# Optimization experiments

Measured on AMD Instinct MI355X. Metric: run time of the kernel, lower is better.

## Reference

```python
import jax, jax.numpy as jnp
import numpy as np

B, S, H = 4, 4096, 768
NB = 16            # n_blocks (first factor)
BSZ = H // NB      # 48, block size
LN_EPS = 1e-12


def setup_inputs() -> dict:
    key = jax.random.key(0)
    ks = jax.random.split(key, 6)
    hidden_states = jax.random.normal(ks[0], (B, S, H), dtype=jnp.float32)
    # Monarch factors: B1 has NB blocks of (BSZ,BSZ); B2 has BSZ blocks of (NB,NB)
    w1_blocks = jax.random.normal(ks[1], (NB, BSZ, BSZ), dtype=jnp.float32) / np.sqrt(BSZ)
    w2_blocks = jax.random.normal(ks[2], (BSZ, NB, NB), dtype=jnp.float32) / np.sqrt(NB)
    gate_w = jax.random.normal(ks[3], (H, H), dtype=jnp.float32) / np.sqrt(H)
    gate_b = jnp.zeros((H,), dtype=jnp.float32)
    out_w = jax.random.normal(ks[4], (H, H), dtype=jnp.float32) / np.sqrt(H)
    out_b = jnp.zeros((H,), dtype=jnp.float32)
    ln_gamma = jnp.ones((H,), dtype=jnp.float32)
    ln_beta = jnp.zeros((H,), dtype=jnp.float32)
    return {
        "hidden_states": hidden_states,
        "w1_blocks": w1_blocks,
        "w2_blocks": w2_blocks,
        "gate_w": gate_w,
        "gate_b": gate_b,
        "out_w": out_w,
        "out_b": out_b,
        "ln_gamma": ln_gamma,
        "ln_beta": ln_beta,
    }


def _monarch(x, w1, w2):
    # x: [B, S, H]; Monarch product P B2 P B1 applied to last dim.
    b, s, h = x.shape
    y = x.reshape(b, s, NB, BSZ)
    y = jnp.einsum('bski,kij->bskj', y, w1)      # block-diag (NB blocks of BSZxBSZ)
    y = jnp.swapaxes(y, -1, -2)                  # permute: [B,S,BSZ,NB]
    y = jnp.einsum('bsqi,qij->bsqj', y, w2)      # block-diag (BSZ blocks of NBxNB)
    y = jnp.swapaxes(y, -1, -2)                  # permute back: [B,S,NB,BSZ]
    return y.reshape(b, s, h)


def _layernorm(x, gamma, beta, eps):
    mu = jnp.mean(x, axis=-1, keepdims=True)
    var = jnp.mean(jnp.square(x - mu), axis=-1, keepdims=True)
    return (x - mu) * jax.lax.rsqrt(var + eps) * gamma + beta


def reference(hidden_states, w1_blocks, w2_blocks, gate_w, gate_b,
              out_w, out_b, ln_gamma, ln_beta):
    residual = hidden_states
    mixed = _monarch(hidden_states, w1_blocks, w2_blocks)
    gate = jax.nn.sigmoid(hidden_states @ gate_w.T + gate_b)
    h = mixed * gate
    h = h @ out_w.T + out_b
    # dropout is identity in eval / p=0
    return _layernorm(h + residual, ln_gamma, ln_beta, LN_EPS)
```

## Files before the change

kernel.cpp:

```cpp
#include <hip/hip_runtime.h>
#include <hip/hip_bf16.h>
#include <stdint.h>

#define HD 768

typedef __attribute__((ext_vector_type(8))) short bf16x8;
typedef __attribute__((ext_vector_type(4))) float f32x4;

__device__ inline unsigned short f2bf(float f) {
  union { float f; unsigned int u; } v; v.f = f;
  return (unsigned short)((v.u + 0x7fffu + ((v.u >> 16) & 1u)) >> 16);
}
__device__ inline float bf2f(unsigned short u) {
  union { unsigned int uu; float f; } v; v.uu = ((unsigned int)u) << 16;
  return v.f;
}

#define LGKM(N) { asm volatile("s_waitcnt lgkmcnt(" #N ")" ::: "memory"); __builtin_amdgcn_sched_barrier(0); }
#define VMC(N) { asm volatile("s_waitcnt vmcnt(" #N ")" ::: "memory"); __builtin_amdgcn_sched_barrier(0); }

__global__ void prep_kernel(const float* __restrict__ gw, const float* __restrict__ ow,
                            const float* __restrict__ w1, const float* __restrict__ w2,
                            unsigned short* __restrict__ Gpk,
                            unsigned short* __restrict__ Opk,
                            unsigned short* __restrict__ w1f,
                            unsigned short* __restrict__ w2f) {
  int bid = blockIdx.x;
  if (bid < 576) {
    const float* src = (bid < 288) ? gw : ow;
    unsigned short* dst = (bid < 288) ? Gpk : Opk;
    int r = ((bid < 288) ? bid : bid - 288) * 256 + threadIdx.x;
    int lane = r & 63;
    int ks = (r >> 6) % 24;
    int nt = r / (24 * 64);
    int n = nt * 16 + (lane & 15);
    int k = ks * 32 + (lane >> 4) * 8;
    bf16x8 pack;
#pragma unroll
    for (int j = 0; j < 8; ++j) pack[j] = (short)f2bf(src[(size_t)n * HD + k + j]);
    *(bf16x8*)(dst + (size_t)r * 8) = pack;
  } else if (bid < 600) {
    int e = (bid - 576) * 256 + threadIdx.x;
    int lane = e & 63, fi = e >> 6;
    int ks = fi & 1, nt = (fi >> 1) % 3, k = fi / 6;
    int lrr = lane & 15, lgg = lane >> 4;
    int q = nt * 16 + lrr;
    bf16x8 pack;
#pragma unroll
    for (int j = 0; j < 8; ++j) {
      int kk = ks * 32 + lgg * 8 + j;
      float v = (kk < 48) ? w1[(k * 48 + kk) * 48 + q] : 0.0f;
      pack[j] = (short)f2bf(v);
    }
    *(bf16x8*)(w1f + (size_t)e * 8) = pack;
  } else {
    int e = (bid - 600) * 256 + threadIdx.x;
    int lane = e & 63, q = e >> 6;
    int lrr = lane & 15, lgg = lane >> 4;
    bf16x8 pack;
#pragma unroll
    for (int j = 0; j < 8; ++j) {
      int kk = lgg * 8 + j;
      float v = (kk < 16) ? w2[(q * 16 + kk) * 16 + lrr] : 0.0f;
      pack[j] = (short)f2bf(v);
    }
    *(bf16x8*)(w2f + (size_t)e * 8) = pack;
  }
}

__global__ __launch_bounds__(512, 1)
void fused_kernel(const float* __restrict__ x,
                  const unsigned short* __restrict__ Gpk,
                  const unsigned short* __restrict__ Opk,
                  const unsigned short* __restrict__ w1f,
                  const unsigned short* __restrict__ w2f,
                  const float* __restrict__ gate_b,
                  const float* __restrict__ out_b,
                  const float* __restrict__ gamma,
                  const float* __restrict__ beta,
                  float* __restrict__ out) {
  __shared__ __align__(16) unsigned char tile[98304];
  __shared__ __align__(16) unsigned char scratch[49152];
  __shared__ float psum[64][8];
  __shared__ float psq[64][8];

  const int tid = threadIdx.x, lane = tid & 63, wid = tid >> 6;
  const int lr = lane & 15, lg = lane >> 4;
  const size_t m0 = (size_t)blockIdx.x * 64;

  float gbv[6], obv[6];
#pragma unroll
  for (int nt = 0; nt < 6; ++nt) {
    int col = wid * 96 + nt * 16 + lr;
    gbv[nt] = gate_b[col];
    obv[nt] = out_b[col];
  }

  {
    const float4* xs = (const float4*)x + m0 * 192;
#pragma unroll
    for (int p = 0; p < 24; ++p) {
      int id = p * 512 + tid;
      float4 v = xs[id];
      int row = id / 192, c4 = id - row * 192;
      uint2 u;
      u.x = (unsigned int)f2bf(v.x) | ((unsigned int)f2bf(v.y) << 16);
      u.y = (unsigned int)f2bf(v.z) | ((unsigned int)f2bf(v.w) << 16);
      *(uint2*)(tile + row * 1536 + ((c4 * 8) ^ ((row & 7) << 4))) = u;
    }
  }
  __syncthreads();

  const int sx0 = (lg * 16) ^ ((lr & 7) << 4);
  const unsigned char* baA0 = tile + lr * 1536 + sx0;
  const unsigned char* baA1 = tile + lr * 1536 + (sx0 ^ 64);
  const unsigned short* gB = Gpk + ((size_t)(wid * 6) * 24 * 64 + lane) * 8;
  const unsigned short* oB = Opk + ((size_t)(wid * 6) * 24 * 64 + lane) * 8;

  bf16x8 aF0[4], aF1[4];
  bf16x8 bP[12], bQ[12];

#define LOAD_B(BB, KT, BR) { _Pragma("unroll") for (int nt = 0; nt < 6; ++nt) { \
      BR[nt * 2 + 0] = *(const bf16x8*)((BB) + nt * 12288 + ((KT) * 2 + 0) * 512); \
      BR[nt * 2 + 1] = *(const bf16x8*)((BB) + nt * 12288 + ((KT) * 2 + 1) * 512); } }
#define RD_A(KT) { _Pragma("unroll") for (int mt = 0; mt < 4; ++mt) { \
      aF0[mt] = *(const bf16x8*)(baA0 + mt * 24576 + (KT) * 128); \
      aF1[mt] = *(const bf16x8*)(baA1 + mt * 24576 + (KT) * 128); } }
#define MM48(ACC, BR) { __builtin_amdgcn_s_setprio(1); \
    _Pragma("unroll") for (int mt = 0; mt < 4; ++mt) \
    _Pragma("unroll") for (int nt = 0; nt < 6; ++nt) { \
      ACC[mt][nt] = __builtin_amdgcn_mfma_f32_16x16x32_bf16(aF0[mt], BR[nt * 2 + 0], ACC[mt][nt], 0, 0, 0); \
      ACC[mt][nt] = __builtin_amdgcn_mfma_f32_16x16x32_bf16(aF1[mt], BR[nt * 2 + 1], ACC[mt][nt], 0, 0, 0); } \
    __builtin_amdgcn_s_setprio(0); }
#define GEMM_LOOP(BB, ACC) { \
    LOAD_B(BB, 0, bP); \
    _Pragma("unroll 1") \
    for (int kt = 0; kt < 10; kt += 2) { \
      LOAD_B(BB, kt + 1, bQ); RD_A(kt); LGKM(0); VMC(12); MM48(ACC, bP); \
      LOAD_B(BB, kt + 2, bP); RD_A(kt + 1); LGKM(0); VMC(12); MM48(ACC, bQ); \
    } \
    LOAD_B(BB, 11, bQ); RD_A(10); LGKM(0); VMC(12); MM48(ACC, bP); \
    RD_A(11); LGKM(0); VMC(0); MM48(ACC, bQ); }

  f32x4 accG[4][6];
#pragma unroll
  for (int mt = 0; mt < 4; ++mt)
#pragma unroll
    for (int nt = 0; nt < 6; ++nt) accG[mt][nt] = (f32x4){0, 0, 0, 0};
  GEMM_LOOP(gB, accG);

  f32x4 accO[4][6];

#define MONARCH_HALF(H) { \
     \
    _Pragma("unroll") for (int kb = 0; kb < 2; ++kb) { \
      const int k = wid * 2 + kb; \
      const unsigned short* wf = w1f + (size_t)(k * 6) * 512 + lane * 8; \
      bf16x8 w1b0 = *(const bf16x8*)(wf + 0 * 512); \
      bf16x8 w1b1 = *(const bf16x8*)(wf + 1 * 512); \
      bf16x8 w1b2 = *(const bf16x8*)(wf + 2 * 512); \
      bf16x8 w1b3 = *(const bf16x8*)(wf + 3 * 512); \
      bf16x8 w1b4 = *(const bf16x8*)(wf + 4 * 512); \
      bf16x8 w1b5 = *(const bf16x8*)(wf + 5 * 512); \
      _Pragma("unroll") for (int mtl = 0; mtl < 2; ++mtl) { \
        const int row = (H) * 32 + mtl * 16 + lr; \
        const int rsw = (lr & 7) << 4; \
        bf16x8 a0 = *(const bf16x8*)(tile + row * 1536 + ((k * 96 + lg * 16) ^ rsw)); \
        bf16x8 a1 = (bf16x8){0, 0, 0, 0, 0, 0, 0, 0}; \
        if (lg < 2) a1 = *(const bf16x8*)(tile + row * 1536 + ((k * 96 + 64 + lg * 16) ^ rsw)); \
        f32x4 c0 = {0,0,0,0}, c1 = {0,0,0,0}, c2 = {0,0,0,0}; \
        c0 = __builtin_amdgcn_mfma_f32_16x16x32_bf16(a0, w1b0, c0, 0, 0, 0); \
        c0 = __builtin_amdgcn_mfma_f32_16x16x32_bf16(a1, w1b1, c0, 0, 0, 0); \
        c1 = __builtin_amdgcn_mfma_f32_16x16x32_bf16(a0, w1b2, c1, 0, 0, 0); \
        c1 = __builtin_amdgcn_mfma_f32_16x16x32_bf16(a1, w1b3, c1, 0, 0, 0); \
        c2 = __builtin_amdgcn_mfma_f32_16x16x32_bf16(a0, w1b4, c2, 0, 0, 0); \
        c2 = __builtin_amdgcn_mfma_f32_16x16x32_bf16(a1, w1b5, c2, 0, 0, 0); \
        _Pragma("unroll") for (int i = 0; i < 4; ++i) { \
          int rl = mtl * 16 + lg * 4 + i; \
          int zsw = (rl & 7) << 4; \
          *(unsigned short*)(scratch + ((rl * 1536 + 0 * 512 + lr * 32 + k * 2) ^ zsw)) = f2bf(c0[i]); \
          *(unsigned short*)(scratch + ((rl * 1536 + 1 * 512 + lr * 32 + k * 2) ^ zsw)) = f2bf(c1[i]); \
          *(unsigned short*)(scratch + ((rl * 1536 + 2 * 512 + lr * 32 + k * 2) ^ zsw)) = f2bf(c2[i]); } } } \
    __syncthreads(); \
     \
    { unsigned int upk[2][4][3]; \
    _Pragma("unroll") for (int qq = 0; qq < 6; ++qq) { \
      const int q = wid * 6 + qq; \
      bf16x8 bw = *(const bf16x8*)(w2f + (size_t)q * 512 + lane * 8); \
      _Pragma("unroll") for (int mtl = 0; mtl < 2; ++mtl) { \
        int rl = mtl * 16 + lr; \
        bf16x8 a = (bf16x8){0, 0, 0, 0, 0, 0, 0, 0}; \
        if (lg < 2) a = *(const bf16x8*)(scratch + ((rl * 1536 + q * 32 + lg * 16) ^ ((rl & 7) << 4))); \
        f32x4 c = {0, 0, 0, 0}; \
        c = __builtin_amdgcn_mfma_f32_16x16x32_bf16(a, bw, c, 0, 0, 0); \
        _Pragma("unroll") for (int i = 0; i < 4; ++i) { \
          unsigned int h = (unsigned int)f2bf(c[i]); \
          if (qq & 1) upk[mtl][i][qq >> 1] |= (h << 16); \
          else        upk[mtl][i][qq >> 1] = h; } } } \
    __syncthreads();   \
     \
    _Pragma("unroll") for (int mtl = 0; mtl < 2; ++mtl) \
    _Pragma("unroll") for (int i = 0; i < 4; ++i) { \
      int rl = mtl * 16 + lg * 4 + i; \
      int base = rl * 1536 + lr * 96 + wid * 12; \
      int msw = (rl & 7) << 4; \
      _Pragma("unroll") for (int p = 0; p < 3; ++p) \
        *(unsigned int*)(scratch + ((base + p * 4) ^ msw)) = upk[mtl][i][p]; } } \
    __syncthreads(); \
     \
    _Pragma("unroll") for (int mtl = 0; mtl < 2; ++mtl) \
    _Pragma("unroll") for (int nt = 0; nt < 6; ++nt) \
    _Pragma("unroll") for (int i = 0; i < 4; ++i) { \
      int rl = mtl * 16 + lg * 4 + i; \
      int row = (H) * 32 + rl; \
      int colb = (wid * 96 + nt * 16 + lr) * 2; \
      float mval = bf2f(*(const unsigned short*)(scratch + ((rl * 1536 + colb) ^ ((rl & 7) << 4)))); \
      float g = accG[(H) * 2 + mtl][nt][i] + gbv[nt]; \
      float s = 1.0f / (1.0f + __expf(-g)); \
      unsigned char* tp = tile + row * 1536 + (colb ^ ((row & 7) << 4)); \
      accO[(H) * 2 + mtl][nt][i] = bf2f(*(const unsigned short*)tp) + obv[nt]; \
      *(unsigned short*)tp = f2bf(s * mval); } \
    __syncthreads(); }

  MONARCH_HALF(0)
  MONARCH_HALF(1)

  GEMM_LOOP(oB, accO);

#pragma unroll
  for (int mt = 0; mt < 4; ++mt) {
#pragma unroll
    for (int i = 0; i < 4; ++i) {
      float s = 0.f, q = 0.f;
#pragma unroll
      for (int nt = 0; nt < 6; ++nt) { float v = accO[mt][nt][i]; s += v; q += v * v; }
#pragma unroll
      for (int off = 8; off >= 1; off >>= 1) {
        s += __shfl_xor(s, off);
        q += __shfl_xor(q, off);
      }
      if (lr == 0) {
        int rl = mt * 16 + lg * 4 + i;
        psum[rl][wid] = s; psq[rl][wid] = q;
      }
    }
  }
  __syncthreads();
#pragma unroll
  for (int mt = 0; mt < 4; ++mt) {
#pragma unroll
    for (int i = 0; i < 4; ++i) {
      int rl = mt * 16 + lg * 4 + i;
      float s = 0.f, q = 0.f;
#pragma unroll
      for (int w = 0; w < 8; ++w) { s += psum[rl][w]; q += psq[rl][w]; }
      float mu = s * (1.0f / 768.0f);
      float var = q * (1.0f / 768.0f) - mu * mu;
      var = var < 0.f ? 0.f : var;
      float rstd = rsqrtf(var + 1e-12f);
      size_t grow = m0 + rl;
#pragma unroll
      for (int nt = 0; nt < 6; ++nt) {
        int col = wid * 96 + nt * 16 + lr;
        out[grow * 768 + col] = (accO[mt][nt][i] - mu) * rstd * gamma[col] + beta[col];
      }
    }
  }
#undef LOAD_B
#undef RD_A
#undef MM48
#undef GEMM_LOOP
#undef MONARCH_HALF
}

extern "C" void kernel_launch(void* const* d_in, const int* in_sizes, int n_in,
                              void* d_out, int out_size, void* d_ws, size_t ws_size,
                              hipStream_t stream) {
  const float* x   = (const float*)d_in[0];
  const float* w1  = (const float*)d_in[1];
  const float* w2  = (const float*)d_in[2];
  const float* gw  = (const float*)d_in[3];
  const float* gb  = (const float*)d_in[4];
  const float* ow  = (const float*)d_in[5];
  const float* ob  = (const float*)d_in[6];
  const float* gam = (const float*)d_in[7];
  const float* bet = (const float*)d_in[8];
  float* out = (float*)d_out;

  char* ws = (char*)d_ws;
  unsigned short* Gpk = (unsigned short*)(ws);
  unsigned short* Opk = (unsigned short*)(ws + 1179648);
  unsigned short* w1f = (unsigned short*)(ws + 2359296);
  unsigned short* w2f = (unsigned short*)(ws + 2457600);

  prep_kernel<<<612, 256, 0, stream>>>(gw, ow, w1, w2, Gpk, Opk, w1f, w2f);
  fused_kernel<<<256, 512, 0, stream>>>(x, Gpk, Opk, w1f, w2f, gb, ob, gam, bet, out);
}
```

Before: 102.8 us.

## Process row block in two halves end-to-end to cut accumulator registers

Restructures the fused kernel to loop over two 32-row halves, running gate GEMM, Monarch mixing, output GEMM and layernorm per half instead of across all 64 rows. This halves the live accumulator arrays, reducing register pressure, and keeps gated activations in scratch rather than overwriting the input tile. In exchange, weight fragments for both dense GEMMs are streamed twice per block and there are additional barriers.

```diff
diff --git a/kernel.cpp b/kernel.cpp
--- a/kernel.cpp
+++ b/kernel.cpp
@@ -81,8 +81,8 @@
                   float* __restrict__ out) {
   __shared__ __align__(16) unsigned char tile[98304];
   __shared__ __align__(16) unsigned char scratch[49152];
-  __shared__ float psum[64][8];
-  __shared__ float psq[64][8];
+  __shared__ float psum[32][8];
+  __shared__ float psq[32][8];
 
   const int tid = threadIdx.x, lane = tid & 63, wid = tid >> 6;
   const int lr = lane & 15, lg = lane >> 4;
@@ -112,165 +112,190 @@
   __syncthreads();
 
   const int sx0 = (lg * 16) ^ ((lr & 7) << 4);
-  const unsigned char* baA0 = tile + lr * 1536 + sx0;
-  const unsigned char* baA1 = tile + lr * 1536 + (sx0 ^ 64);
   const unsigned short* gB = Gpk + ((size_t)(wid * 6) * 24 * 64 + lane) * 8;
   const unsigned short* oB = Opk + ((size_t)(wid * 6) * 24 * 64 + lane) * 8;
 
-  bf16x8 aF0[4], aF1[4];
+  bf16x8 aF0[2], aF1[2];
   bf16x8 bP[12], bQ[12];
 
 #define LOAD_B(BB, KT, BR) { _Pragma("unroll") for (int nt = 0; nt < 6; ++nt) { \
       BR[nt * 2 + 0] = *(const bf16x8*)((BB) + nt * 12288 + ((KT) * 2 + 0) * 512); \
       BR[nt * 2 + 1] = *(const bf16x8*)((BB) + nt * 12288 + ((KT) * 2 + 1) * 512); } }
-#define RD_A(KT) { _Pragma("unroll") for (int mt = 0; mt < 4; ++mt) { \
-      aF0[mt] = *(const bf16x8*)(baA0 + mt * 24576 + (KT) * 128); \
-      aF1[mt] = *(const bf16x8*)(baA1 + mt * 24576 + (KT) * 128); } }
-#define MM48(ACC, BR) { __builtin_amdgcn_s_setprio(1); \
-    _Pragma("unroll") for (int mt = 0; mt < 4; ++mt) \
+#define RD_A(BA0, BA1, KT) { _Pragma("unroll") for (int mt = 0; mt < 2; ++mt) { \
+      aF0[mt] = *(const bf16x8*)((BA0) + mt * 24576 + (KT) * 128); \
+      aF1[mt] = *(const bf16x8*)((BA1) + mt * 24576 + (KT) * 128); } }
+#define MM24(ACC, BR) { __builtin_amdgcn_s_setprio(1); \
+    _Pragma("unroll") for (int mt = 0; mt < 2; ++mt) \
     _Pragma("unroll") for (int nt = 0; nt < 6; ++nt) { \
       ACC[mt][nt] = __builtin_amdgcn_mfma_f32_16x16x32_bf16(aF0[mt], BR[nt * 2 + 0], ACC[mt][nt], 0, 0, 0); \
       ACC[mt][nt] = __builtin_amdgcn_mfma_f32_16x16x32_bf16(aF1[mt], BR[nt * 2 + 1], ACC[mt][nt], 0, 0, 0); } \
     __builtin_amdgcn_s_setprio(0); }
-#define GEMM_LOOP(BB, ACC) { \
+#define GEMM_LOOP(BB, ACC, BA0, BA1) { \
     LOAD_B(BB, 0, bP); \
     _Pragma("unroll 1") \
     for (int kt = 0; kt < 10; kt += 2) { \
-      LOAD_B(BB, kt + 1, bQ); RD_A(kt); LGKM(0); VMC(12); MM48(ACC, bP); \
-      LOAD_B(BB, kt + 2, bP); RD_A(kt + 1); LGKM(0); VMC(12); MM48(ACC, bQ); \
+      LOAD_B(BB, kt + 1, bQ); RD_A(BA0, BA1, kt); LGKM(0); VMC(12); MM24(ACC, bP); \
+      LOAD_B(BB, kt + 2, bP); RD_A(BA0, BA1, kt + 1); LGKM(0); VMC(12); MM24(ACC, bQ); \
     } \
-    LOAD_B(BB, 11, bQ); RD_A(10); LGKM(0); VMC(12); MM48(ACC, bP); \
-    RD_A(11); LGKM(0); VMC(0); MM48(ACC, bQ); }
-
-  f32x4 accG[4][6];
-#pragma unroll
-  for (int mt = 0; mt < 4; ++mt)
-#pragma unroll
-    for (int nt = 0; nt < 6; ++nt) accG[mt][nt] = (f32x4){0, 0, 0, 0};
-  GEMM_LOOP(gB, accG);
-
-  f32x4 accO[4][6];
-
-#define MONARCH_HALF(H) { \
-     \
-    _Pragma("unroll") for (int kb = 0; kb < 2; ++kb) { \
-      const int k = wid * 2 + kb; \
-      const unsigned short* wf = w1f + (size_t)(k * 6) * 512 + lane * 8; \
-      bf16x8 w1b0 = *(const bf16x8*)(wf + 0 * 512); \
-      bf16x8 w1b1 = *(const bf16x8*)(wf + 1 * 512); \
-      bf16x8 w1b2 = *(const bf16x8*)(wf + 2 * 512); \
-      bf16x8 w1b3 = *(const bf16x8*)(wf + 3 * 512); \
-      bf16x8 w1b4 = *(const bf16x8*)(wf + 4 * 512); \
-      bf16x8 w1b5 = *(const bf16x8*)(wf + 5 * 512); \
-      _Pragma("unroll") for (int mtl = 0; mtl < 2; ++mtl) { \
-        const int row = (H) * 32 + mtl * 16 + lr; \
-        const int rsw = (lr & 7) << 4; \
-        bf16x8 a0 = *(const bf16x8*)(tile + row * 1536 + ((k * 96 + lg * 16) ^ rsw)); \
-        bf16x8 a1 = (bf16x8){0, 0, 0, 0, 0, 0, 0, 0}; \
-        if (lg < 2) a1 = *(const bf16x8*)(tile + row * 1536 + ((k * 96 + 64 + lg * 16) ^ rsw)); \
-        f32x4 c0 = {0,0,0,0}, c1 = {0,0,0,0}, c2 = {0,0,0,0}; \
-        c0 = __builtin_amdgcn_mfma_f32_16x16x32_bf16(a0, w1b0, c0, 0, 0, 0); \
-        c0 = __builtin_amdgcn_mfma_f32_16x16x32_bf16(a1, w1b1, c0, 0, 0, 0); \
-        c1 = __builtin_amdgcn_mfma_f32_16x16x32_bf16(a0, w1b2, c1, 0, 0, 0); \
-        c1 = __builtin_amdgcn_mfma_f32_16x16x32_bf16(a1, w1b3, c1, 0, 0, 0); \
-        c2 = __builtin_amdgcn_mfma_f32_16x16x32_bf16(a0, w1b4, c2, 0, 0, 0); \
-        c2 = __builtin_amdgcn_mfma_f32_16x16x32_bf16(a1, w1b5, c2, 0, 0, 0); \
-        _Pragma("unroll") for (int i = 0; i < 4; ++i) { \
-          int rl = mtl * 16 + lg * 4 + i; \
-          int zsw = (rl & 7) << 4; \
-          *(unsigned short*)(scratch + ((rl * 1536 + 0 * 512 + lr * 32 + k * 2) ^ zsw)) = f2bf(c0[i]); \
-          *(unsigned short*)(scratch + ((rl * 1536 + 1 * 512 + lr * 32 + k * 2) ^ zsw)) = f2bf(c1[i]); \
-          *(unsigned short*)(scratch + ((rl * 1536 + 2 * 512 + lr * 32 + k * 2) ^ zsw)) = f2bf(c2[i]); } } } \
-    __syncthreads(); \
-     \
-    { unsigned int upk[2][4][3]; \
-    _Pragma("unroll") for (int qq = 0; qq < 6; ++qq) { \
-      const int q = wid * 6 + qq; \
-      bf16x8 bw = *(const bf16x8*)(w2f + (size_t)q * 512 + lane * 8); \
-      _Pragma("unroll") for (int mtl = 0; mtl < 2; ++mtl) { \
-        int rl = mtl * 16 + lr; \
-        bf16x8 a = (bf16x8){0, 0, 0, 0, 0, 0, 0, 0}; \
-        if (lg < 2) a = *(const bf16x8*)(scratch + ((rl * 1536 + q * 32 + lg * 16) ^ ((rl & 7) << 4))); \
-        f32x4 c = {0, 0, 0, 0}; \
-        c = __builtin_amdgcn_mfma_f32_16x16x32_bf16(a, bw, c, 0, 0, 0); \
-        _Pragma("unroll") for (int i = 0; i < 4; ++i) { \
-          unsigned int h = (unsigned int)f2bf(c[i]); \
-          if (qq & 1) upk[mtl][i][qq >> 1] |= (h << 16); \
-          else        upk[mtl][i][qq >> 1] = h; } } } \
-    __syncthreads();   \
-     \
-    _Pragma("unroll") for (int mtl = 0; mtl < 2; ++mtl) \
-    _Pragma("unroll") for (int i = 0; i < 4; ++i) { \
-      int rl = mtl * 16 + lg * 4 + i; \
-      int base = rl * 1536 + lr * 96 + wid * 12; \
-      int msw = (rl & 7) << 4; \
-      _Pragma("unroll") for (int p = 0; p < 3; ++p) \
-        *(unsigned int*)(scratch + ((base + p * 4) ^ msw)) = upk[mtl][i][p]; } } \
-    __syncthreads(); \
-     \
-    _Pragma("unroll") for (int mtl = 0; mtl < 2; ++mtl) \
-    _Pragma("unroll") for (int nt = 0; nt < 6; ++nt) \
-    _Pragma("unroll") for (int i = 0; i < 4; ++i) { \
-      int rl = mtl * 16 + lg * 4 + i; \
-      int row = (H) * 32 + rl; \
-      int colb = (wid * 96 + nt * 16 + lr) * 2; \
-      float mval = bf2f(*(const unsigned short*)(scratch + ((rl * 1536 + colb) ^ ((rl & 7) << 4)))); \
-      float g = accG[(H) * 2 + mtl][nt][i] + gbv[nt]; \
-      float s = 1.0f / (1.0f + __expf(-g)); \
-      unsigned char* tp = tile + row * 1536 + (colb ^ ((row & 7) << 4)); \
-      accO[(H) * 2 + mtl][nt][i] = bf2f(*(const unsigned short*)tp) + obv[nt]; \
-      *(unsigned short*)tp = f2bf(s * mval); } \
-    __syncthreads(); }
-
-  MONARCH_HALF(0)
-  MONARCH_HALF(1)
-
-  GEMM_LOOP(oB, accO);
-
-#pragma unroll
-  for (int mt = 0; mt < 4; ++mt) {
-#pragma unroll
-    for (int i = 0; i < 4; ++i) {
-      float s = 0.f, q = 0.f;
-#pragma unroll
-      for (int nt = 0; nt < 6; ++nt) { float v = accO[mt][nt][i]; s += v; q += v * v; }
-#pragma unroll
-      for (int off = 8; off >= 1; off >>= 1) {
-        s += __shfl_xor(s, off);
-        q += __shfl_xor(q, off);
-      }
-      if (lr == 0) {
+    LOAD_B(BB, 11, bQ); RD_A(BA0, BA1, 10); LGKM(0); VMC(12); MM24(ACC, bP); \
+    RD_A(BA0, BA1, 11); LGKM(0); VMC(0); MM24(ACC, bQ); }
+
+#pragma unroll 1
+  for (int H = 0; H < 2; ++H) {
+    const int hb0 = H * 32;
+
+    f32x4 accG[2][6];
+#pragma unroll
+    for (int mt = 0; mt < 2; ++mt)
+#pragma unroll
+      for (int nt = 0; nt < 6; ++nt) accG[mt][nt] = (f32x4){0, 0, 0, 0};
+    {
+      const unsigned char* xA0 = tile + (hb0 + lr) * 1536 + sx0;
+      const unsigned char* xA1 = tile + (hb0 + lr) * 1536 + (sx0 ^ 64);
+      GEMM_LOOP(gB, accG, xA0, xA1);
+    }
+
+#pragma unroll
+    for (int kb = 0; kb < 2; ++kb) {
+      const int k = wid * 2 + kb;
+      const unsigned short* wf = w1f + (size_t)(k * 6) * 512 + lane * 8;
+      bf16x8 w1b0 = *(const bf16x8*)(wf + 0 * 512);
+      bf16x8 w1b1 = *(const bf16x8*)(wf + 1 * 512);
+      bf16x8 w1b2 = *(const bf16x8*)(wf + 2 * 512);
+      bf16x8 w1b3 = *(const bf16x8*)(wf + 3 * 512);
+      bf16x8 w1b4 = *(const bf16x8*)(wf + 4 * 512);
+      bf16x8 w1b5 = *(const bf16x8*)(wf + 5 * 512);
+#pragma unroll
+      for (int mtl = 0; mtl < 2; ++mtl) {
+        const int row = hb0 + mtl * 16 + lr;
+        const int rsw = (lr & 7) << 4;
+        bf16x8 a0 = *(const bf16x8*)(tile + row * 1536 + ((k * 96 + lg * 16) ^ rsw));
+        bf16x8 a1 = (bf16x8){0, 0, 0, 0, 0, 0, 0, 0};
+        if (lg < 2) a1 = *(const bf16x8*)(tile + row * 1536 + ((k * 96 + 64 + lg * 16) ^ rsw));
+        f32x4 c0 = {0, 0, 0, 0}, c1 = {0, 0, 0, 0}, c2 = {0, 0, 0, 0};
+        c0 = __builtin_amdgcn_mfma_f32_16x16x32_bf16(a0, w1b0, c0, 0, 0, 0);
+        c0 = __builtin_amdgcn_mfma_f32_16x16x32_bf16(a1, w1b1, c0, 0, 0, 0);
+        c1 = __builtin_amdgcn_mfma_f32_16x16x32_bf16(a0, w1b2, c1, 0, 0, 0);
+        c1 = __builtin_amdgcn_mfma_f32_16x16x32_bf16(a1, w1b3, c1, 0, 0, 0);
+        c2 = __builtin_amdgcn_mfma_f32_16x16x32_bf16(a0, w1b4, c2, 0, 0, 0);
+        c2 = __builtin_amdgcn_mfma_f32_16x16x32_bf16(a1, w1b5, c2, 0, 0, 0);
+#pragma unroll
+        for (int i = 0; i < 4; ++i) {
+          int rl = mtl * 16 + lg * 4 + i;
+          int zsw = (rl & 7) << 4;
+          *(unsigned short*)(scratch + ((rl * 1536 + 0 * 512 + lr * 32 + k * 2) ^ zsw)) = f2bf(c0[i]);
+          *(unsigned short*)(scratch + ((rl * 1536 + 1 * 512 + lr * 32 + k * 2) ^ zsw)) = f2bf(c1[i]);
+          *(unsigned short*)(scratch + ((rl * 1536 + 2 * 512 + lr * 32 + k * 2) ^ zsw)) = f2bf(c2[i]);
+        }
+      }
+    }
+    __syncthreads();
+
+    unsigned int upk[2][4][3];
+#pragma unroll
+    for (int qq = 0; qq < 6; ++qq) {
+      const int q = wid * 6 + qq;
+      bf16x8 bw = *(const bf16x8*)(w2f + (size_t)q * 512 + lane * 8);
+#pragma unroll
+      for (int mtl = 0; mtl < 2; ++mtl) {
+        int rl = mtl * 16 + lr;
+        bf16x8 a = (bf16x8){0, 0, 0, 0, 0, 0, 0, 0};
+        if (lg < 2) a = *(const bf16x8*)(scratch + ((rl * 1536 + q * 32 + lg * 16) ^ ((rl & 7) << 4)));
+        f32x4 c = {0, 0, 0, 0};
+        c = __builtin_amdgcn_mfma_f32_16x16x32_bf16(a, bw, c, 0, 0, 0);
+#pragma unroll
+        for (int i = 0; i < 4; ++i) {
+          unsigned int h = (unsigned int)f2bf(c[i]);
+          if (qq & 1) upk[mtl][i][qq >> 1] |= (h << 16);
+          else        upk[mtl][i][qq >> 1] = h;
+        }
+      }
+    }
+    __syncthreads();
+
+#pragma unroll
+    for (int mtl = 0; mtl < 2; ++mtl)
+#pragma unroll
+      for (int i = 0; i < 4; ++i) {
+        int rl = mtl * 16 + lg * 4 + i;
+        int base = rl * 1536 + lr * 96 + wid * 12;
+        int msw = (rl & 7) << 4;
+#pragma unroll
+        for (int p = 0; p < 3; ++p)
+          *(unsigned int*)(scratch + ((base + p * 4) ^ msw)) = upk[mtl][i][p];
+      }
+    __syncthreads();
+
+    f32x4 accO[2][6];
+#pragma unroll
+    for (int mtl = 0; mtl < 2; ++mtl)
+#pragma unroll
+      for (int nt = 0; nt < 6; ++nt)
+#pragma unroll
+        for (int i = 0; i < 4; ++i) {
+          int rl = mtl * 16 + lg * 4 + i;
+          int row = hb0 + rl;
+          int colb = (wid * 96 + nt * 16 + lr) * 2;
+          unsigned char* sp = scratch + ((rl * 1536 + colb) ^ ((rl & 7) << 4));
+          float mval = bf2f(*(const unsigned short*)sp);
+          float g = accG[mtl][nt][i] + gbv[nt];
+          float s = 1.0f / (1.0f + __expf(-g));
+          accO[mtl][nt][i] = bf2f(*(const unsigned short*)(tile + row * 1536 + (colb ^ ((row & 7) << 4)))) + obv[nt];
+          *(unsigned short*)sp = f2bf(s * mval);
+        }
+    __syncthreads();
+
+    {
+      const unsigned char* hA0 = scratch + lr * 1536 + sx0;
+      const unsigned char* hA1 = scratch + lr * 1536 + (sx0 ^ 64);
+      GEMM_LOOP(oB, accO, hA0, hA1);
+    }
+
+#pragma unroll
+    for (int mt = 0; mt < 2; ++mt) {
+#pragma unroll
+      for (int i = 0; i < 4; ++i) {
+        float s = 0.f, q = 0.f;
+#pragma unroll
+        for (int nt = 0; nt < 6; ++nt) { float v = accO[mt][nt][i]; s += v; q += v * v; }
+#pragma unroll
+        for (int off = 8; off >= 1; off >>= 1) {
+          s += __shfl_xor(s, off);
+          q += __shfl_xor(q, off);
+        }
+        if (lr == 0) {
+          int rl = mt * 16 + lg * 4 + i;
+          psum[rl][wid] = s; psq[rl][wid] = q;
+        }
+      }
+    }
+    __syncthreads();
+#pragma unroll
+    for (int mt = 0; mt < 2; ++mt) {
+#pragma unroll
+      for (int i = 0; i < 4; ++i) {
         int rl = mt * 16 + lg * 4 + i;
-        psum[rl][wid] = s; psq[rl][wid] = q;
-      }
-    }
-  }
-  __syncthreads();
-#pragma unroll
-  for (int mt = 0; mt < 4; ++mt) {
-#pragma unroll
-    for (int i = 0; i < 4; ++i) {
-      int rl = mt * 16 + lg * 4 + i;
-      float s = 0.f, q = 0.f;
-#pragma unroll
-      for (int w = 0; w < 8; ++w) { s += psum[rl][w]; q += psq[rl][w]; }
-      float mu = s * (1.0f / 768.0f);
-      float var = q * (1.0f / 768.0f) - mu * mu;
-      var = var < 0.f ? 0.f : var;
-      float rstd = rsqrtf(var + 1e-12f);
-      size_t grow = m0 + rl;
-#pragma unroll
-      for (int nt = 0; nt < 6; ++nt) {
-        int col = wid * 96 + nt * 16 + lr;
-        out[grow * 768 + col] = (accO[mt][nt][i] - mu) * rstd * gamma[col] + beta[col];
-      }
-    }
+        float s = 0.f, q = 0.f;
+#pragma unroll
+        for (int w = 0; w < 8; ++w) { s += psum[rl][w]; q += psq[rl][w]; }
+        float mu = s * (1.0f / 768.0f);
+        float var = q * (1.0f / 768.0f) - mu * mu;
+        var = var < 0.f ? 0.f : var;
+        float rstd = rsqrtf(var + 1e-12f);
+        size_t grow = m0 + hb0 + rl;
+#pragma unroll
+        for (int nt = 0; nt < 6; ++nt) {
+          int col = wid * 96 + nt * 16 + lr;
+          out[grow * 768 + col] = (accO[mt][nt][i] - mu) * rstd * gamma[col] + beta[col];
+        }
+      }
+    }
+    __syncthreads();
   }
 #undef LOAD_B
 #undef RD_A
-#undef MM48
+#undef MM24
 #undef GEMM_LOOP
-#undef MONARCH_HALF
 }
 
 extern "C" void kernel_launch(void* const* d_in, const int* in_sizes, int n_in,
```

After: 191.1 us. 1.86x slower.
